# Kernel optimization log

Measured on AMD Instinct MI355X. Metric: run time of the kernel, lower is better.

## Reference

```python
import jax, jax.numpy as jnp
import numpy as np

D_MODEL = 1024
NUM_HEADS = 16
D_K = D_MODEL // NUM_HEADS


def setup_inputs() -> dict:
    key = jax.random.key(0)
    ks = jax.random.split(key, 11)
    B, S = 2, 2048
    scale = 1.0 / np.sqrt(D_MODEL)
    inp = {
        'q': jax.random.normal(ks[0], (B, S, D_MODEL), jnp.float32),
        'k': jax.random.normal(ks[1], (B, S, D_MODEL), jnp.float32),
        'v': jax.random.normal(ks[2], (B, S, D_MODEL), jnp.float32),
        'Wq': jax.random.normal(ks[3], (D_MODEL, D_MODEL), jnp.float32) * scale,
        'bq': jnp.zeros((D_MODEL,), jnp.float32),
        'Wk': jax.random.normal(ks[4], (D_MODEL, D_MODEL), jnp.float32) * scale,
        'bk': jnp.zeros((D_MODEL,), jnp.float32),
        'Wv': jax.random.normal(ks[5], (D_MODEL, D_MODEL), jnp.float32) * scale,
        'bv': jnp.zeros((D_MODEL,), jnp.float32),
        'Wo': jax.random.normal(ks[6], (D_MODEL, D_MODEL), jnp.float32) * scale,
        'bo': jnp.zeros((D_MODEL,), jnp.float32),
    }
    return inp


def _split_heads(x):
    # [B, S, d_model] -> [B, H, S, d_k]
    B, S, _ = x.shape
    return x.reshape(B, S, NUM_HEADS, D_K).transpose(0, 2, 1, 3)


def reference(q, k, v, Wq, bq, Wk, bk, Wv, bv, Wo, bo):
    B, S, _ = q.shape
    qh = _split_heads(q @ Wq + bq)
    kh = _split_heads(k @ Wk + bk)
    vh = _split_heads(v @ Wv + bv)
    scores = jnp.einsum('bhsd,bhtd->bhst', qh, kh) / np.sqrt(D_K)
    attn = jax.nn.softmax(scores, axis=-1)  # dropout is identity in eval
    out = jnp.einsum('bhst,bhtd->bhsd', attn, vh)
    out = out.transpose(0, 2, 1, 3).reshape(B, S, D_MODEL)
    return out @ Wo + bo
```

## Files before the change

kernel.cpp:

```cpp
#include <hip/hip_runtime.h>

typedef unsigned short u16;
typedef unsigned int u32;
typedef __attribute__((ext_vector_type(4))) float f32x4;
typedef __attribute__((ext_vector_type(16))) float f32x16;
typedef __attribute__((ext_vector_type(8))) short bf16x8;
typedef __attribute__((ext_vector_type(4))) unsigned short u16x4;
typedef __attribute__((ext_vector_type(8))) unsigned short u16x8;
typedef __attribute__((ext_vector_type(4))) unsigned int u32x4;

#define S_LEN 2048
#define DMODEL 1024

__device__ __forceinline__ u16 f2bf(float f) {
  union { float f; unsigned int i; } c; c.f = f;
  unsigned int v = c.i + 0x7FFFu + ((c.i >> 16) & 1u);
  return (u16)(v >> 16);
}
__device__ __forceinline__ u32 cvtpk(float lo, float hi) {
  u32 r;
  asm("v_cvt_pk_bf16_f32 %0, %1, %2" : "=v"(r) : "v"(lo), "v"(hi));
  return r;
}
__device__ __forceinline__ float exp2v(float x) {
  float r;
  asm("v_exp_f32 %0, %1" : "=v"(r) : "v"(x));
  return r;
}

typedef const __attribute__((address_space(1))) void gv_t;
typedef __attribute__((address_space(3))) void lv_t;
__device__ __forceinline__ void gload_lds16(const void* g, void* l) {
  __builtin_amdgcn_global_load_lds((gv_t*)g, (lv_t*)l, 16, 0, 0);
}

struct TwArgs { const float* src[4]; u16* dst[4]; };
__global__ __launch_bounds__(256) void k_twcvt4(TwArgs ta) {
  __shared__ u16 tile[64][68];
  int wsel = blockIdx.x >> 8;
  int bx = blockIdx.x & 255;
  const float* src = ta.src[wsel];
  u16* dst = ta.dst[wsel];
  const int R = 1024, C = 1024;
  int tr = bx >> 4, tc = bx & 15;
  int r0 = tr << 6, c0 = tc << 6;
  int t = threadIdx.x;
#pragma unroll
  for (int i = 0; i < 4; ++i) {
    int e = (t + i * 256) << 2;
    int rr = e >> 6, cc = e & 63;
    f32x4 v = *(const f32x4*)&src[(size_t)(r0 + rr) * C + (c0 + cc)];
#pragma unroll
    for (int j = 0; j < 4; ++j) tile[rr][cc + j] = f2bf(v[j]);
  }
  __syncthreads();
#pragma unroll
  for (int i = 0; i < 4; ++i) {
    int e = (t + i * 256) << 2;
    int rr = e >> 6, cc = e & 63;
    u16x4 v;
#pragma unroll
    for (int j = 0; j < 4; ++j) v[j] = tile[cc + j][rr];
    *(u16x4*)&dst[(size_t)(c0 + rr) * R + (r0 + cc)] = v;
  }
}

__global__ __launch_bounds__(256) void k_pack(const u16* __restrict__ Ck,
                                              const u16* __restrict__ Cv,
                                              u16* __restrict__ Kp,
                                              u16* __restrict__ Vp) {
  int bx = blockIdx.x;
  if (bx < 2048) {
    int flat = bx * 256 + threadIdx.x;
    int lane = flat & 63, kd = (flat >> 6) & 3, kt = (flat >> 8) & 63;
    int h = (flat >> 14) & 15, b = flat >> 18;
    int l31 = lane & 31, hi = lane >> 5;
    const u16* src = &Ck[(size_t)(b * 2048 + kt * 32 + l31) * 1024 + h * 64 + kd * 16 + hi * 8];
    ((u16x8*)Kp)[flat] = *(const u16x8*)src;
  } else {
    int flat = (bx - 2048) * 256 + threadIdx.x;
    int lane = flat & 63, ks = (flat >> 6) & 3, dvh = (flat >> 8) & 1;
    int kt = (flat >> 9) & 31, h = (flat >> 14) & 15, b = flat >> 18;
    int l31 = lane & 31, hi = lane >> 5;
    const u16* src = &Cv[(size_t)(b * 2048 + kt * 64 + ks * 16 + hi * 8) * 1024 + h * 64 + dvh * 32 + l31];
    u16x8 o;
#pragma unroll
    for (int j = 0; j < 8; ++j) o[j] = src[(size_t)j * 1024];
    ((u16x8*)Vp)[flat] = o;
  }
}

struct GemmSet { const void* A; const u16* Bt; const float* bias; void* C; };
struct GemmArgs { GemmSet s[3]; };

template <int AF32, int OUTF32>
__global__ __launch_bounds__(256) void k_gemm_bt(GemmArgs ga) {
  constexpr int K = 1024, N = 1024;
  __shared__ __align__(16) u16 Al[128 * 32];
  __shared__ __align__(16) u16 Bl[128 * 32];
  int mat = blockIdx.x >> 8;
  int t = blockIdx.x & 255;
  int m0 = (t & 31) << 7;
  int n0 = (t >> 5) << 7;
  const u16* Bt = ga.s[mat].Bt;
  int lane = threadIdx.x & 63, w = threadIdx.x >> 6;
  int g = lane >> 4, cl = lane & 15;
  int wr = w >> 1, wc = w & 1;
  f32x4 zero4 = {0.f, 0.f, 0.f, 0.f};
  f32x4 acc[4][4];
#pragma unroll
  for (int i = 0; i < 4; ++i)
#pragma unroll
    for (int j = 0; j < 4; ++j) acc[i][j] = zero4;

  int srow0 = w * 32 + (lane >> 2);
  int scol = (lane & 3) << 3;
  for (int kt = 0; kt < K / 32; ++kt) {
    int k0 = kt << 5;
#pragma unroll
    for (int c = 0; c < 2; ++c) {
      int row = srow0 + c * 16;
      if (AF32) {
        const float* Af = (const float*)ga.s[mat].A;
        const float* ap = &Af[(size_t)(m0 + row) * K + k0 + scol];
        f32x4 u0 = *(const f32x4*)ap;
        f32x4 u1 = *(const f32x4*)(ap + 4);
        union { u32x4 u; } pk;
        pk.u = u32x4{cvtpk(u0[0], u0[1]), cvtpk(u0[2], u0[3]),
                     cvtpk(u1[0], u1[1]), cvtpk(u1[2], u1[3])};
        *(u32x4*)&Al[w * 1024 + c * 512 + lane * 8] = pk.u;
      } else {
        const u16* Ab = (const u16*)ga.s[mat].A;
        gload_lds16(&Ab[(size_t)(m0 + row) * K + k0 + scol], &Al[w * 1024 + c * 512]);
      }
      gload_lds16(&Bt[(size_t)(n0 + row) * K + k0 + scol], &Bl[w * 1024 + c * 512]);
    }
    __syncthreads();
    bf16x8 af[4], bfm[4];
#pragma unroll
    for (int i = 0; i < 4; ++i) {
      af[i]  = *(const bf16x8*)&Al[(wr * 64 + i * 16 + cl) * 32 + g * 8];
      bfm[i] = *(const bf16x8*)&Bl[(wc * 64 + i * 16 + cl) * 32 + g * 8];
    }
#pragma unroll
    for (int mi = 0; mi < 4; ++mi)
#pragma unroll
      for (int ni = 0; ni < 4; ++ni)
        acc[mi][ni] = __builtin_amdgcn_mfma_f32_16x16x32_bf16(af[mi], bfm[ni], acc[mi][ni], 0, 0, 0);
    __syncthreads();
  }
  const float* bias = ga.s[mat].bias;
#pragma unroll
  for (int ni = 0; ni < 4; ++ni) {
    int n = n0 + wc * 64 + ni * 16 + cl;
    float bv = bias[n];
#pragma unroll
    for (int mi = 0; mi < 4; ++mi) {
      int r0 = m0 + wr * 64 + mi * 16 + g * 4;
#pragma unroll
      for (int r = 0; r < 4; ++r) {
        float val = acc[mi][ni][r] + bv;
        if (OUTF32) ((float*)ga.s[mat].C)[(size_t)(r0 + r) * N + n] = val;
        else        ((u16*)ga.s[mat].C)[(size_t)(r0 + r) * N + n] = f2bf(val);
      }
    }
  }
}

__global__ __launch_bounds__(256, 4) void k_attn5(const u16* __restrict__ Q,
                                                  const u16* __restrict__ Kp,
                                                  const u16* __restrict__ Vp,
                                                  u16* __restrict__ O) {
  __shared__ __align__(16) float Ol[2][32][64];
  __shared__ float Ml[2][32];
  int lane = threadIdx.x & 63, w = threadIdx.x >> 6;
  int l31 = lane & 31, hi = lane >> 5;
  int half = w >> 1, sub = w & 1;
  int bx = blockIdx.x;
  int logical = (bx & 7) * 128 + (bx >> 3);
  int bh = logical >> 5, qblk = logical & 31;
  int b = bh >> 4, h = bh & 15;
  const u16* Qb = Q + (size_t)b * S_LEN * DMODEL + h * 64;
  const u16* Kph = Kp + (size_t)(b * 16 + h) * (64 * 4 * 64 * 8);
  const u16* Vph = Vp + (size_t)(b * 16 + h) * (32 * 2 * 4 * 64 * 8);
  u16* Ob = O + (size_t)b * S_LEN * DMODEL + h * 64;
  int qbase = qblk * 64 + sub * 32;

  bf16x8 qf[4];
  const u16* qp = &Qb[(size_t)(qbase + l31) * DMODEL + hi * 8];
#pragma unroll
  for (int kd = 0; kd < 4; ++kd) qf[kd] = *(const bf16x8*)&qp[kd * 16];

  f32x16 zero16 = {0};
  f32x16 oa0 = zero16, oa1 = zero16;
  float lsum = 0.f;
  const float C2 = 0.125f * 1.44269504f;
  const float MC2 = 64.0f * C2;

  int kt0 = half * 16;
  for (int kt = kt0; kt < kt0 + 16; ++kt) {
    const u16* kpt = Kph + (size_t)kt * 4096 + (size_t)lane * 8;
    const u16* vpt = Vph + (size_t)kt * 4096 + (size_t)lane * 8;

    f32x16 s0 = zero16, s1 = zero16;
    __builtin_amdgcn_s_setprio(1);
#pragma unroll
    for (int kd = 0; kd < 4; ++kd) {
      bf16x8 kfa = *(const bf16x8*)&kpt[kd * 512];
      bf16x8 kfb = *(const bf16x8*)&kpt[2048 + kd * 512];
      s0 = __builtin_amdgcn_mfma_f32_32x32x16_bf16(kfa, qf[kd], s0, 0, 0, 0);
      s1 = __builtin_amdgcn_mfma_f32_32x32x16_bf16(kfb, qf[kd], s1, 0, 0, 0);
    }
    __builtin_amdgcn_s_setprio(0);

    bf16x8 vf0[4], vf1[4];
#pragma unroll
    for (int ks = 0; ks < 4; ++ks) {
      vf0[ks] = *(const bf16x8*)&vpt[ks * 512];
      vf1[ks] = *(const bf16x8*)&vpt[2048 + ks * 512];
    }

    float rs = 0.f;
    bf16x8 af[4];
#pragma unroll
    for (int tile = 0; tile < 2; ++tile) {
      const f32x16& sv = tile ? s1 : s0;
#pragma unroll
      for (int hq = 0; hq < 2; ++hq) {
        float p0 = exp2v(__builtin_fmaf(sv[hq * 8 + 0], C2, -MC2));
        float p1 = exp2v(__builtin_fmaf(sv[hq * 8 + 1], C2, -MC2));
        rs += p0 + p1;
        u32 w0 = cvtpk(p0, p1);
        p0 = exp2v(__builtin_fmaf(sv[hq * 8 + 2], C2, -MC2));
        p1 = exp2v(__builtin_fmaf(sv[hq * 8 + 3], C2, -MC2));
        rs += p0 + p1;
        u32 w1 = cvtpk(p0, p1);
        p0 = exp2v(__builtin_fmaf(sv[hq * 8 + 4], C2, -MC2));
        p1 = exp2v(__builtin_fmaf(sv[hq * 8 + 5], C2, -MC2));
        rs += p0 + p1;
        u32 w2 = cvtpk(p0, p1);
        p0 = exp2v(__builtin_fmaf(sv[hq * 8 + 6], C2, -MC2));
        p1 = exp2v(__builtin_fmaf(sv[hq * 8 + 7], C2, -MC2));
        rs += p0 + p1;
        u32 w3 = cvtpk(p0, p1);
        u32 x0 = __shfl_xor(w0, 32, 64), x1 = __shfl_xor(w1, 32, 64);
        u32 x2 = __shfl_xor(w2, 32, 64), x3 = __shfl_xor(w3, 32, 64);
        union { u32x4 u; bf16x8 v; } c;
        c.u = u32x4{hi ? x2 : w0, hi ? x3 : w1, hi ? w2 : x0, hi ? w3 : x1};
        af[tile * 2 + hq] = c.v;
      }
    }
    lsum += rs + __shfl_xor(rs, 32, 64);

    __builtin_amdgcn_s_setprio(1);
#pragma unroll
    for (int ks = 0; ks < 4; ++ks) {
      oa0 = __builtin_amdgcn_mfma_f32_32x32x16_bf16(af[ks], vf0[ks], oa0, 0, 0, 0);
      oa1 = __builtin_amdgcn_mfma_f32_32x32x16_bf16(af[ks], vf1[ks], oa1, 0, 0, 0);
    }
    __builtin_amdgcn_s_setprio(0);
  }

  if (half == 1) {
#pragma unroll
    for (int r = 0; r < 16; ++r) {
      int q = ((r & 3) + 8 * (r >> 2)) + 4 * hi;
      Ol[sub][q][l31] = oa0[r];
      Ol[sub][q][l31 + 32] = oa1[r];
    }
    if (hi == 0) Ml[sub][l31] = lsum;
  }
  __syncthreads();
  if (half == 0) {
    float invl = 1.0f / (lsum + Ml[sub][l31]);
#pragma unroll
    for (int r = 0; r < 16; ++r) {
      int q = ((r & 3) + 8 * (r >> 2)) + 4 * hi;
      float f0 = __shfl(invl, q, 64);
      int row = qbase + q;
      float o0 = (oa0[r] + Ol[sub][q][l31]) * f0;
      float o1 = (oa1[r] + Ol[sub][q][l31 + 32]) * f0;
      Ob[(size_t)row * DMODEL + l31]      = f2bf(o0);
      Ob[(size_t)row * DMODEL + 32 + l31] = f2bf(o1);
    }
  }
}

extern "C" void kernel_launch(void* const* d_in, const int* in_sizes, int n_in,
                              void* d_out, int out_size, void* d_ws, size_t ws_size,
                              hipStream_t stream) {
  const float* q  = (const float*)d_in[0];
  const float* k  = (const float*)d_in[1];
  const float* v  = (const float*)d_in[2];
  const float* Wq = (const float*)d_in[3];
  const float* bq = (const float*)d_in[4];
  const float* Wk = (const float*)d_in[5];
  const float* bk = (const float*)d_in[6];
  const float* Wv = (const float*)d_in[7];
  const float* bv = (const float*)d_in[8];
  const float* Wo = (const float*)d_in[9];
  const float* bo = (const float*)d_in[10];
  float* out = (float*)d_out;
  char* ws = (char*)d_ws;
  const size_t MB = 1024 * 1024;
  u16* wtq = (u16*)(ws + 0 * MB);
  u16* wtk = (u16*)(ws + 2 * MB);
  u16* wtv = (u16*)(ws + 4 * MB);
  u16* wto = (u16*)(ws + 6 * MB);
  u16* Kp  = (u16*)(ws + 8 * MB);
  u16* O   = (u16*)(ws + 16 * MB);
  u16* Vp  = (u16*)(ws + 24 * MB);
  u16* Cq  = (u16*)(ws + 32 * MB);
  u16* Ck  = (u16*)(ws + 40 * MB);
  u16* Cv  = (u16*)(ws + 48 * MB);

  TwArgs ta;
  ta.src[0] = Wq; ta.src[1] = Wk; ta.src[2] = Wv; ta.src[3] = Wo;
  ta.dst[0] = wtq; ta.dst[1] = wtk; ta.dst[2] = wtv; ta.dst[3] = wto;
  k_twcvt4<<<1024, 256, 0, stream>>>(ta);

  GemmArgs ga;
  ga.s[0] = {q, wtq, bq, (void*)Cq};
  ga.s[1] = {k, wtk, bk, (void*)Ck};
  ga.s[2] = {v, wtv, bv, (void*)Cv};
  k_gemm_bt<1, 0><<<768, 256, 0, stream>>>(ga);

  k_pack<<<4096, 256, 0, stream>>>(Ck, Cv, Kp, Vp);

  k_attn5<<<1024, 256, 0, stream>>>(Cq, Kp, Vp, O);

  GemmArgs go;
  go.s[0] = {O, wto, bo, (void*)out};
  go.s[1] = go.s[0];
  go.s[2] = go.s[0];
  k_gemm_bt<0, 1><<<256, 256, 0, stream>>>(go);
}
```

Baseline: 281.3 us.

## Pre-convert activations to bf16 and use 256x256 pipelined QKV GEMM

Adds a separate kernel that converts q, k and v to bf16 up front, so the QKV projection GEMM can load A directly into LDS asynchronously. The projection kernel is replaced by a 512-thread GEMM with 256x256 tiles, double-buffered and XOR-swizzled LDS, explicit waitcnt/barrier scheduling and raised MFMA priority, which increases data reuse and overlaps loads with compute. The cost is an extra launch and extra memory traffic for the converted activations. The 192-block grid may also underfill the GPU's compute units.

```diff
diff --git a/kernel.cpp b/kernel.cpp
--- a/kernel.cpp
+++ b/kernel.cpp
@@ -32,6 +32,28 @@
 typedef __attribute__((address_space(3))) void lv_t;
 __device__ __forceinline__ void gload_lds16(const void* g, void* l) {
   __builtin_amdgcn_global_load_lds((gv_t*)g, (lv_t*)l, 16, 0, 0);
+}
+
+#define LGKM0 do { asm volatile("s_waitcnt lgkmcnt(0)" ::: "memory"); __builtin_amdgcn_sched_barrier(0); } while (0)
+#define VMC4  do { asm volatile("s_waitcnt vmcnt(4)" ::: "memory"); __builtin_amdgcn_sched_barrier(0); } while (0)
+#define BAR   __builtin_amdgcn_s_barrier()
+
+__global__ __launch_bounds__(256) void k_cvt3(const float* __restrict__ s0,
+                                              const float* __restrict__ s1,
+                                              const float* __restrict__ s2,
+                                              u16* __restrict__ d0,
+                                              u16* __restrict__ d1,
+                                              u16* __restrict__ d2) {
+  int i = blockIdx.x * 256 + threadIdx.x;
+  int seg = i >> 19, idx = i & 524287;
+  const float* s = seg == 0 ? s0 : (seg == 1 ? s1 : s2);
+  u16* d = seg == 0 ? d0 : (seg == 1 ? d1 : d2);
+  f32x4 a = ((const f32x4*)s)[idx * 2];
+  f32x4 b = ((const f32x4*)s)[idx * 2 + 1];
+  u16x8 o;
+#pragma unroll
+  for (int j = 0; j < 4; ++j) { o[j] = f2bf(a[j]); o[j + 4] = f2bf(b[j]); }
+  ((u16x8*)d)[idx] = o;
 }
 
 struct TwArgs { const float* src[4]; u16* dst[4]; };
@@ -90,19 +112,144 @@
   }
 }
 
-struct GemmSet { const void* A; const u16* Bt; const float* bias; void* C; };
+struct GemmSet { const u16* A; const u16* Bt; const float* bias; void* C; };
 struct GemmArgs { GemmSet s[3]; };
 
-template <int AF32, int OUTF32>
-__global__ __launch_bounds__(256) void k_gemm_bt(GemmArgs ga) {
+template <int MB>
+__device__ __forceinline__ void quad16(f32x4 (&acc)[8][4], const bf16x8 (&Af)[4],
+                                       const bf16x8 (&Bf)[4]) {
+#pragma unroll
+  for (int mi = 0; mi < 4; ++mi)
+#pragma unroll
+    for (int nf = 0; nf < 4; ++nf)
+      acc[MB + mi][nf] = __builtin_amdgcn_mfma_f32_16x16x32_bf16(Af[mi], Bf[nf],
+                                                                 acc[MB + mi][nf], 0, 0, 0);
+}
+template <int MB>
+__device__ __forceinline__ void rda4(bf16x8 (&Af)[4], const char* base, const int (&aoff)[8]) {
+#pragma unroll
+  for (int mi = 0; mi < 4; ++mi) Af[mi] = *(const bf16x8*)(base + aoff[MB + mi]);
+}
+__device__ __forceinline__ void rdb4(bf16x8 (&Bf)[4], const char* base, const int (&boff)[4]) {
+#pragma unroll
+  for (int nf = 0; nf < 4; ++nf) Bf[nf] = *(const bf16x8*)(base + boff[nf]);
+}
+
+__global__ __launch_bounds__(512, 2) void k_gemm8(GemmArgs ga) {
+  __shared__ __align__(16) u16 lds[2][2][2][256 * 32];
+  int tid = threadIdx.x;
+  int lane = tid & 63, w = tid >> 6;
+  int cl = lane & 15, g = lane >> 4;
+  int wr = w >> 2, wc = w & 3;
+  int wgs = ((blockIdx.x & 7) * 24) + (blockIdx.x >> 3);
+  int mat = wgs >> 6;
+  int rr = wgs & 63;
+  int m0 = (rr >> 2) << 8, n0 = (rr & 3) << 8;
+  const u16* A = ga.s[mat].A;
+  const u16* Bt = ga.s[mat].Bt;
+
+  int srow[2], scol[2];
+#pragma unroll
+  for (int i = 0; i < 2; ++i) {
+    int c = tid + i * 512;
+    int cp = c ^ (((c >> 5) & 3) << 1);
+    srow[i] = cp >> 2;
+    scol[i] = (cp & 3) * 8;
+  }
+  int aoff[8], boff[4];
+#pragma unroll
+  for (int mf = 0; mf < 8; ++mf) {
+    int x = (wr * 128 + mf * 16 + cl) * 64 + g * 16;
+    aoff[mf] = x ^ (((x >> 9) & 3) << 5);
+  }
+#pragma unroll
+  for (int nf = 0; nf < 4; ++nf) {
+    int x = (wc * 64 + nf * 16 + cl) * 64 + g * 16;
+    boff[nf] = x ^ (((x >> 9) & 3) << 5);
+  }
+
+  f32x4 acc[8][4];
+  f32x4 z4 = {0.f, 0.f, 0.f, 0.f};
+#pragma unroll
+  for (int i = 0; i < 8; ++i)
+#pragma unroll
+    for (int j = 0; j < 4; ++j) acc[i][j] = z4;
+
+  auto STAGE = [&](int u, int ab, int hk) {
+    int k0 = (u << 6) + (hk << 5);
+    const u16* src = ab ? Bt : A;
+    int rb = ab ? n0 : m0;
+    u16* dst = &lds[u & 1][ab][hk][0];
+#pragma unroll
+    for (int i = 0; i < 2; ++i)
+      gload_lds16(&src[(size_t)(rb + srow[i]) * 1024 + k0 + scol[i]],
+                  &dst[(w * 64 + i * 512) * 8]);
+  };
+
+  STAGE(0, 0, 0); STAGE(0, 1, 0); STAGE(0, 0, 1); STAGE(0, 1, 1);
+  VMC4;
+  BAR;
+
+  bf16x8 Af[4], Bf[4];
+#pragma unroll 2
+  for (int t = 0; t < 16; ++t) {
+    int d = t & 1;
+    int u = t + 1;
+    bool st = u < 16;
+    const char* Ah0 = (const char*)&lds[d][0][0][0];
+    const char* Bh0 = (const char*)&lds[d][1][0][0];
+    const char* Ah1 = (const char*)&lds[d][0][1][0];
+    const char* Bh1 = (const char*)&lds[d][1][1][0];
+    rda4<0>(Af, Ah0, aoff); rdb4(Bf, Bh0, boff);
+    if (st) STAGE(u, 0, 0);
+    BAR; LGKM0;
+    __builtin_amdgcn_s_setprio(1); quad16<0>(acc, Af, Bf); __builtin_amdgcn_s_setprio(0);
+    BAR;
+    rda4<4>(Af, Ah0, aoff);
+    if (st) STAGE(u, 1, 0);
+    BAR; LGKM0;
+    __builtin_amdgcn_s_setprio(1); quad16<4>(acc, Af, Bf); __builtin_amdgcn_s_setprio(0);
+    VMC4;
+    BAR;
+    rda4<0>(Af, Ah1, aoff); rdb4(Bf, Bh1, boff);
+    if (st) STAGE(u, 0, 1);
+    BAR; LGKM0;
+    __builtin_amdgcn_s_setprio(1); quad16<0>(acc, Af, Bf); __builtin_amdgcn_s_setprio(0);
+    BAR;
+    rda4<4>(Af, Ah1, aoff);
+    if (st) STAGE(u, 1, 1);
+    BAR; LGKM0;
+    __builtin_amdgcn_s_setprio(1); quad16<4>(acc, Af, Bf); __builtin_amdgcn_s_setprio(0);
+    VMC4;
+    BAR;
+  }
+
+  const float* bias = ga.s[mat].bias;
+  u16* C = (u16*)ga.s[mat].C;
+#pragma unroll
+  for (int nf = 0; nf < 4; ++nf) {
+    int n = n0 + wc * 64 + nf * 16 + cl;
+    float bv = bias[n];
+#pragma unroll
+    for (int mf = 0; mf < 8; ++mf) {
+      int row0 = m0 + wr * 128 + mf * 16 + g * 4;
+#pragma unroll
+      for (int j = 0; j < 4; ++j)
+        C[(size_t)(row0 + j) * 1024 + n] = f2bf(acc[mf][nf][j] + bv);
+    }
+  }
+}
+
+__global__ __launch_bounds__(256) void k_gemm_out(const u16* __restrict__ A,
+                                                  const u16* __restrict__ Bt,
+                                                  const float* __restrict__ bias,
+                                                  float* __restrict__ C) {
   constexpr int K = 1024, N = 1024;
   __shared__ __align__(16) u16 Al[128 * 32];
   __shared__ __align__(16) u16 Bl[128 * 32];
-  int mat = blockIdx.x >> 8;
-  int t = blockIdx.x & 255;
+  int t = blockIdx.x;
   int m0 = (t & 31) << 7;
   int n0 = (t >> 5) << 7;
-  const u16* Bt = ga.s[mat].Bt;
   int lane = threadIdx.x & 63, w = threadIdx.x >> 6;
   int g = lane >> 4, cl = lane & 15;
   int wr = w >> 1, wc = w & 1;
@@ -120,19 +267,7 @@
 #pragma unroll
     for (int c = 0; c < 2; ++c) {
       int row = srow0 + c * 16;
-      if (AF32) {
-        const float* Af = (const float*)ga.s[mat].A;
-        const float* ap = &Af[(size_t)(m0 + row) * K + k0 + scol];
-        f32x4 u0 = *(const f32x4*)ap;
-        f32x4 u1 = *(const f32x4*)(ap + 4);
-        union { u32x4 u; } pk;
-        pk.u = u32x4{cvtpk(u0[0], u0[1]), cvtpk(u0[2], u0[3]),
-                     cvtpk(u1[0], u1[1]), cvtpk(u1[2], u1[3])};
-        *(u32x4*)&Al[w * 1024 + c * 512 + lane * 8] = pk.u;
-      } else {
-        const u16* Ab = (const u16*)ga.s[mat].A;
-        gload_lds16(&Ab[(size_t)(m0 + row) * K + k0 + scol], &Al[w * 1024 + c * 512]);
-      }
+      gload_lds16(&A[(size_t)(m0 + row) * K + k0 + scol], &Al[w * 1024 + c * 512]);
       gload_lds16(&Bt[(size_t)(n0 + row) * K + k0 + scol], &Bl[w * 1024 + c * 512]);
     }
     __syncthreads();
@@ -149,7 +284,6 @@
         acc[mi][ni] = __builtin_amdgcn_mfma_f32_16x16x32_bf16(af[mi], bfm[ni], acc[mi][ni], 0, 0, 0);
     __syncthreads();
   }
-  const float* bias = ga.s[mat].bias;
 #pragma unroll
   for (int ni = 0; ni < 4; ++ni) {
     int n = n0 + wc * 64 + ni * 16 + cl;
@@ -158,11 +292,8 @@
     for (int mi = 0; mi < 4; ++mi) {
       int r0 = m0 + wr * 64 + mi * 16 + g * 4;
 #pragma unroll
-      for (int r = 0; r < 4; ++r) {
-        float val = acc[mi][ni][r] + bv;
-        if (OUTF32) ((float*)ga.s[mat].C)[(size_t)(r0 + r) * N + n] = val;
-        else        ((u16*)ga.s[mat].C)[(size_t)(r0 + r) * N + n] = f2bf(val);
-      }
+      for (int r = 0; r < 4; ++r)
+        C[(size_t)(r0 + r) * N + n] = acc[mi][ni][r] + bv;
     }
   }
 }
@@ -307,12 +438,17 @@
   u16* wtk = (u16*)(ws + 2 * MB);
   u16* wtv = (u16*)(ws + 4 * MB);
   u16* wto = (u16*)(ws + 6 * MB);
-  u16* Kp  = (u16*)(ws + 8 * MB);
-  u16* O   = (u16*)(ws + 16 * MB);
-  u16* Vp  = (u16*)(ws + 24 * MB);
+  u16* qb  = (u16*)(ws + 8 * MB);
+  u16* kb  = (u16*)(ws + 16 * MB);
+  u16* vb  = (u16*)(ws + 24 * MB);
   u16* Cq  = (u16*)(ws + 32 * MB);
   u16* Ck  = (u16*)(ws + 40 * MB);
   u16* Cv  = (u16*)(ws + 48 * MB);
+  u16* Kp  = qb;
+  u16* Vp  = vb;
+  u16* O   = kb;
+
+  k_cvt3<<<6144, 256, 0, stream>>>(q, k, v, qb, kb, vb);
 
   TwArgs ta;
   ta.src[0] = Wq; ta.src[1] = Wk; ta.src[2] = Wv; ta.src[3] = Wo;
@@ -320,18 +456,14 @@
   k_twcvt4<<<1024, 256, 0, stream>>>(ta);
 
   GemmArgs ga;
-  ga.s[0] = {q, wtq, bq, (void*)Cq};
-  ga.s[1] = {k, wtk, bk, (void*)Ck};
-  ga.s[2] = {v, wtv, bv, (void*)Cv};
-  k_gemm_bt<1, 0><<<768, 256, 0, stream>>>(ga);
+  ga.s[0] = {qb, wtq, bq, (void*)Cq};
+  ga.s[1] = {kb, wtk, bk, (void*)Ck};
+  ga.s[2] = {vb, wtv, bv, (void*)Cv};
+  k_gemm8<<<192, 512, 0, stream>>>(ga);
 
   k_pack<<<4096, 256, 0, stream>>>(Ck, Cv, Kp, Vp);
 
   k_attn5<<<1024, 256, 0, stream>>>(Cq, Kp, Vp, O);
 
-  GemmArgs go;
-  go.s[0] = {O, wto, bo, (void*)out};
-  go.s[1] = go.s[0];
-  go.s[2] = go.s[0];
-  k_gemm_bt<0, 1><<<256, 256, 0, stream>>>(go);
-}
+  k_gemm_out<<<256, 256, 0, stream>>>(O, wto, bo, out);
+}
```

New measurement: 246.1 us. -12.5%, faster.
